# Optimization experiments

Measured on AMD Instinct MI355X. Metric: run time of the kernel, lower is better.

## Reference

```python
import jax, jax.numpy as jnp
import numpy as np

THETA0 = 3.0
THETA = 5.0


def _edt(bg):
    """Exact Euclidean distance transform.
    bg: [B,H,W] bool, True where distance is 0 (the 'background'/feature set).
    Returns [B,H,W] float32 distance of every pixel to the nearest True pixel.
    Separable two-pass algorithm: 1D pass along H via scan, then exact
    min over column offsets along W (Meijster lower-envelope done densely).
    """
    B, H, W = bg.shape
    big = jnp.float32(H + W)
    f = bg.astype(jnp.float32)
    xs = jnp.moveaxis(f, 1, 0)  # [H,B,W] scan over rows

    def step(carry, row):
        d = jnp.where(row > 0, 0.0, carry + 1.0)
        return d, d

    init = jnp.full((B, W), big, jnp.float32)
    _, gf = jax.lax.scan(step, init, xs)                  # top-down
    _, gb = jax.lax.scan(step, init, xs, reverse=True)    # bottom-up
    g = jnp.minimum(gf, gb)            # [H,B,W] 1D vertical distance
    g = jnp.moveaxis(g, 0, 1)          # [B,H,W]
    g2 = jnp.minimum(g, big) ** 2
    col = jnp.arange(W, dtype=jnp.float32)
    off2 = (col[:, None] - col[None, :]) ** 2             # [j,k]
    # d2[b,i,j] = min_k g2[b,i,k] + (j-k)^2   -> [B,H,W,W] intermediate
    d2 = jnp.min(g2[:, :, None, :] + off2[None, None, :, :], axis=-1)
    return jnp.sqrt(d2)


def reference(predictions, targets):
    # predictions: [B,1,H,W] logits; targets: [B,1,H,W] binary masks
    t = targets[:, 0]                                   # [B,H,W]
    fg = t > 0.5
    dist_pos = _edt(~fg)   # distance_transform_edt(target): dist to nearest 0
    dist_neg = _edt(fg)    # distance_transform_edt(1-target): dist to nearest 1
    dist_map = jnp.where(fg, dist_pos, -dist_neg)
    # weight = 1 / (1 + exp((|d| - theta0)/theta)) == sigmoid(-(|d|-theta0)/theta)
    weight = jax.nn.sigmoid(-(jnp.abs(dist_map) - THETA0) / THETA)[:, None]  # [B,1,H,W]
    # numerically stable BCE-with-logits == BCE(sigmoid(x), t)
    x = predictions
    bce = jnp.maximum(x, 0.0) - x * targets + jnp.log1p(jnp.exp(-jnp.abs(x)))
    return jnp.mean(bce * weight)


def setup_inputs() -> dict:
    key = jax.random.key(0)
    k1, k2 = jax.random.split(key)
    B, C, H, W = 8, 1, 256, 256
    predictions = jax.random.normal(k1, (B, C, H, W), dtype=jnp.float32)
    targets = jax.random.randint(k2, (B, C, H, W), 0, 2).astype(jnp.float32)
    return {"predictions": predictions, "targets": targets}
```

## Files before the change

kernel.cpp:

```cpp
#include <hip/hip_runtime.h>
#include <math.h>

#define BB 8
#define HH 256
#define WW 256
#define NPIX (BB*HH*WW)
#define BIGI 512
#define BIGBIG (1<<20)

#define P_OFF   (2 * NPIX)
#define P_STRIDE 32
#define C_OFF   (P_OFF + 16 * P_STRIDE)

__global__ __launch_bounds__(512) void pack_masks_t(
    const float* __restrict__ tgt,
    float* __restrict__ ws) {
  __shared__ unsigned int halfw[2][8][32];

  if (blockIdx.x == 0) {
    if (threadIdx.x < 16) ws[P_OFF + threadIdx.x * P_STRIDE] = 0.0f;
    if (threadIdx.x == 16) ((int*)ws)[C_OFF] = 0;
  }

  int tid = threadIdx.x;
  int h = tid >> 8;
  int j = (tid >> 5) & 7;
  int c = tid & 31;
  int im = blockIdx.x >> 3;
  int w = ((blockIdx.x & 7) << 5) + c;
  size_t ib = (size_t)im * (HH * WW) + (size_t)(32 * j + 16 * h) * WW + w;

  unsigned int m = 0;
#pragma unroll
  for (int i = 0; i < 16; ++i) {
    float t = tgt[ib + (size_t)i * WW];
    m |= (t > 0.5f ? 1u : 0u) << i;
  }
  halfw[h][j][c] = m;
  __syncthreads();

  if (h == 0) {
    unsigned int full = halfw[0][j][c] | (halfw[1][j][c] << 16);
    ((unsigned int*)ws)[im * 2048 + w * 8 + j] = full;
  }
}

#define ENV_G(gg) { float4 v = s4[gg];                            \
    float D0 = fw - (float)((gg) << 2);                           \
    d2 = fminf(d2, fmaf(D0, D0, v.x));                            \
    float D1 = D0 - 1.0f; d2 = fminf(d2, fmaf(D1, D1, v.y));      \
    float D2 = D0 - 2.0f; d2 = fminf(d2, fmaf(D2, D2, v.z));      \
    float D3 = D0 - 3.0f; d2 = fminf(d2, fmaf(D3, D3, v.w)); }

__global__ __launch_bounds__(1024) void edt_row_loss5(
    const float* __restrict__ pred,
    float* __restrict__ ws,
    float* __restrict__ out) {
  __shared__ __align__(16) float lA[4][WW];
  __shared__ __align__(16) float lB[4][WW];
  __shared__ float wsum[16];
  __shared__ int lastFlag;

  const unsigned int* maskws = (const unsigned int*)ws;
  float* partials = ws + P_OFF;
  int* counter = ((int*)ws) + C_OFF;

  int tid = threadIdx.x;
  int im = blockIdx.x >> 6;
  int rg = blockIdx.x & 63;
  int r = tid >> 8;
  int w = tid & 255;
  int R = 4 * rg + r;
  int k = R >> 5;
  int rr = R & 31;

  const uint4* mp = (const uint4*)(maskws + im * 2048 + w * 8);
  uint4 mlo = mp[0], mhi = mp[1];
  unsigned int M[8] = {mlo.x, mlo.y, mlo.z, mlo.w, mhi.x, mhi.y, mhi.z, mhi.w};

  float x = pred[(size_t)blockIdx.x * (4 * WW) + tid];

  int fcA = BIGBIG, fcB = BIGBIG, bcA = BIGBIG, bcB = BIGBIG;
  {
    int cA = BIGBIG, cB = BIGBIG;
#pragma unroll
    for (int j = 0; j < 8; ++j) {
      if (j == k) { fcA = cA; fcB = cB; }
      unsigned int a = ~M[j], bm = M[j];
      cA = a  ? (int)__builtin_clz(a)  : cA + 32;
      cB = bm ? (int)__builtin_clz(bm) : cB + 32;
    }
  }
  {
    int cA = BIGBIG, cB = BIGBIG;
#pragma unroll
    for (int j = 7; j >= 0; --j) {
      if (j == k) { bcA = cA; bcB = cB; }
      unsigned int a = ~M[j], bm = M[j];
      cA = a  ? (int)__builtin_ctz(a)  : cA + 32;
      cB = bm ? (int)__builtin_ctz(bm) : cB + 32;
    }
  }

  unsigned int mk = M[k];
  bool fg = (mk >> rr) & 1u;
  float t = fg ? 1.0f : 0.0f;

  {
    unsigned int mA = ~mk;
    unsigned int xx = mA << (31 - rr);
    unsigned int yy = mA >> rr;
    int df = xx ? (int)__builtin_clz(xx) : (rr + 1 + fcA);
    int db = yy ? (int)__builtin_ctz(yy) : (32 - rr + bcA);
    int d = min(min(df, db), BIGI);
    lA[r][w] = (float)(d * d);
  }
  {
    unsigned int xx = mk << (31 - rr);
    unsigned int yy = mk >> rr;
    int df = xx ? (int)__builtin_clz(xx) : (rr + 1 + fcB);
    int db = yy ? (int)__builtin_ctz(yy) : (32 - rr + bcB);
    int d = min(min(df, db), BIGI);
    lB[r][w] = (float)(d * d);
  }
  __syncthreads();

  const float4* s4 = (const float4*)(fg ? lA[r] : lB[r]);
  int gc = w >> 2;
  float fw = (float)w;
  float d2 = 1e30f;

  ENV_G(gc);
  for (int dlt = 1; dlt <= 16; ++dlt) {
    int gl = gc - dlt, gr = gc + dlt;
    int bl = (gl >= 0) ? (w - 4 * gl - 3) : 100000;
    int br = (gr <= 63) ? (4 * gr - w) : 100000;
    int bb = min(bl, br);
    float bb2 = (float)bb * (float)bb;
    if (__all(d2 <= bb2)) break;
    if (gl >= 0) ENV_G(gl);
    if (gr <= 63) ENV_G(gr);
  }

  float dd = sqrtf(d2);
  float weight = 1.0f / (1.0f + __expf((dd - 3.0f) * 0.2f));
  float bce = fmaxf(x, 0.0f) - x * t + log1pf(__expf(-fabsf(x)));
  float c = bce * weight * (1.0f / (float)NPIX);

#pragma unroll
  for (int off = 32; off > 0; off >>= 1) c += __shfl_down(c, off, 64);
  if ((tid & 63) == 0) wsum[tid >> 6] = c;
  __syncthreads();

  if (tid < 64) {
    float v = (tid < 16) ? wsum[tid] : 0.0f;
#pragma unroll
    for (int off = 8; off > 0; off >>= 1) v += __shfl_down(v, off, 64);
    if (tid == 0) {
      atomicAdd(&partials[(blockIdx.x & 15) * P_STRIDE], v);
      __threadfence();
      int done = atomicAdd(counter, 1);
      lastFlag = (done == (int)gridDim.x - 1) ? 1 : 0;
    }
  }
  __syncthreads();

  if (lastFlag && tid < 64) {
    float v = (tid < 16) ? atomicAdd(&partials[tid * P_STRIDE], 0.0f) : 0.0f;
#pragma unroll
    for (int off = 8; off > 0; off >>= 1) v += __shfl_down(v, off, 64);
    if (tid == 0) out[0] = v;
  }
}

extern "C" void kernel_launch(void* const* d_in, const int* in_sizes, int n_in,
                              void* d_out, int out_size, void* d_ws, size_t ws_size,
                              hipStream_t stream) {
  const float* pred = (const float*)d_in[0];
  const float* tgt  = (const float*)d_in[1];
  float* out = (float*)d_out;
  float* ws  = (float*)d_ws;

  pack_masks_t<<<dim3(64), dim3(512), 0, stream>>>(tgt, ws);
  edt_row_loss5<<<dim3(512), dim3(1024), 0, stream>>>(pred, ws, out);
}
```

Baseline: 69.90 us.

## Process four rows per thread in EDT kernel and widen mask packing grid

The EDT/loss kernel now has each thread handle four rows of one column, using 512-thread blocks and half as many blocks, so the per-column mask scans and loads are amortised across four rows and there is more independent work per thread. The packing kernel splits each 32-row word into four 8-row chunks across twice as many blocks to raise parallelism on the target reads. The cost is more registers per thread and fewer total threads, and the early-exit vote now waits for all four rows, which can add envelope iterations.

```diff
diff --git a/kernel.cpp b/kernel.cpp
--- a/kernel.cpp
+++ b/kernel.cpp
@@ -12,10 +12,10 @@
 #define P_STRIDE 32
 #define C_OFF   (P_OFF + 16 * P_STRIDE)
 
-__global__ __launch_bounds__(512) void pack_masks_t(
+__global__ __launch_bounds__(512) void pack_masks_t2(
     const float* __restrict__ tgt,
     float* __restrict__ ws) {
-  __shared__ unsigned int halfw[2][8][32];
+  __shared__ unsigned int chunk[4][4][32];
 
   if (blockIdx.x == 0) {
     if (threadIdx.x < 16) ws[P_OFF + threadIdx.x * P_STRIDE] = 0.0f;
@@ -23,42 +23,49 @@
   }
 
   int tid = threadIdx.x;
-  int h = tid >> 8;
-  int j = (tid >> 5) & 7;
-  int c = tid & 31;
-  int im = blockIdx.x >> 3;
-  int w = ((blockIdx.x & 7) << 5) + c;
-  size_t ib = (size_t)im * (HH * WW) + (size_t)(32 * j + 16 * h) * WW + w;
+  int c  = tid & 31;
+  int jl = (tid >> 5) & 3;
+  int h  = tid >> 7;
+  int im = blockIdx.x >> 4;
+  int tl = (blockIdx.x >> 1) & 7;
+  int v  = blockIdx.x & 1;
+  int j  = 4 * v + jl;
+  int w  = (tl << 5) + c;
+  size_t ib = (size_t)im * (HH * WW) + (size_t)(32 * j + 8 * h) * WW + w;
 
   unsigned int m = 0;
 #pragma unroll
-  for (int i = 0; i < 16; ++i) {
+  for (int i = 0; i < 8; ++i) {
     float t = tgt[ib + (size_t)i * WW];
     m |= (t > 0.5f ? 1u : 0u) << i;
   }
-  halfw[h][j][c] = m;
+  chunk[h][jl][c] = m;
   __syncthreads();
 
   if (h == 0) {
-    unsigned int full = halfw[0][j][c] | (halfw[1][j][c] << 16);
+    unsigned int full = chunk[0][jl][c] | (chunk[1][jl][c] << 8) |
+                        (chunk[2][jl][c] << 16) | (chunk[3][jl][c] << 24);
     ((unsigned int*)ws)[im * 2048 + w * 8 + j] = full;
   }
 }
 
-#define ENV_G(gg) { float4 v = s4[gg];                            \
-    float D0 = fw - (float)((gg) << 2);                           \
-    d2 = fminf(d2, fmaf(D0, D0, v.x));                            \
-    float D1 = D0 - 1.0f; d2 = fminf(d2, fmaf(D1, D1, v.y));      \
-    float D2 = D0 - 2.0f; d2 = fminf(d2, fmaf(D2, D2, v.z));      \
-    float D3 = D0 - 3.0f; d2 = fminf(d2, fmaf(D3, D3, v.w)); }
-
-__global__ __launch_bounds__(1024) void edt_row_loss5(
+__device__ __forceinline__ void env4(const float4* __restrict__ s4, int gg,
+                                     float fw, float& d2) {
+  float4 v = s4[gg];
+  float D0 = fw - (float)(gg << 2);
+  d2 = fminf(d2, fmaf(D0, D0, v.x));
+  float D1 = D0 - 1.0f; d2 = fminf(d2, fmaf(D1, D1, v.y));
+  float D2 = D0 - 2.0f; d2 = fminf(d2, fmaf(D2, D2, v.z));
+  float D3 = D0 - 3.0f; d2 = fminf(d2, fmaf(D3, D3, v.w));
+}
+
+__global__ __launch_bounds__(512) void edt_row_loss7(
     const float* __restrict__ pred,
     float* __restrict__ ws,
     float* __restrict__ out) {
-  __shared__ __align__(16) float lA[4][WW];
-  __shared__ __align__(16) float lB[4][WW];
-  __shared__ float wsum[16];
+  __shared__ __align__(16) float lA[8][WW];
+  __shared__ __align__(16) float lB[8][WW];
+  __shared__ float wsum[8];
   __shared__ int lastFlag;
 
   const unsigned int* maskws = (const unsigned int*)ws;
@@ -66,26 +73,34 @@
   int* counter = ((int*)ws) + C_OFF;
 
   int tid = threadIdx.x;
-  int im = blockIdx.x >> 6;
-  int rg = blockIdx.x & 63;
+  int bid = blockIdx.x;
+  int im = bid >> 5;
+  int rg = bid & 31;
   int r = tid >> 8;
   int w = tid & 255;
-  int R = 4 * rg + r;
-  int k = R >> 5;
-  int rr = R & 31;
+  int R0 = 8 * rg + 4 * r;
+
+  int kq[4], rq[4];
+#pragma unroll
+  for (int p = 0; p < 4; ++p) { kq[p] = (R0 + p) >> 5; rq[p] = (R0 + p) & 31; }
 
   const uint4* mp = (const uint4*)(maskws + im * 2048 + w * 8);
   uint4 mlo = mp[0], mhi = mp[1];
   unsigned int M[8] = {mlo.x, mlo.y, mlo.z, mlo.w, mhi.x, mhi.y, mhi.z, mhi.w};
 
-  float x = pred[(size_t)blockIdx.x * (4 * WW) + tid];
-
-  int fcA = BIGBIG, fcB = BIGBIG, bcA = BIGBIG, bcB = BIGBIG;
+  size_t pb = (size_t)bid * 2048 + (size_t)r * 1024 + w;
+  float x[4];
+#pragma unroll
+  for (int p = 0; p < 4; ++p) x[p] = pred[pb + (size_t)(p << 8)];
+
+  int fcA[4], fcB[4], bcA[4], bcB[4];
   {
     int cA = BIGBIG, cB = BIGBIG;
 #pragma unroll
     for (int j = 0; j < 8; ++j) {
-      if (j == k) { fcA = cA; fcB = cB; }
+#pragma unroll
+      for (int p = 0; p < 4; ++p)
+        if (j == kq[p]) { fcA[p] = cA; fcB[p] = cB; }
       unsigned int a = ~M[j], bm = M[j];
       cA = a  ? (int)__builtin_clz(a)  : cA + 32;
       cB = bm ? (int)__builtin_clz(bm) : cB + 32;
@@ -95,57 +110,78 @@
     int cA = BIGBIG, cB = BIGBIG;
 #pragma unroll
     for (int j = 7; j >= 0; --j) {
-      if (j == k) { bcA = cA; bcB = cB; }
+#pragma unroll
+      for (int p = 0; p < 4; ++p)
+        if (j == kq[p]) { bcA[p] = cA; bcB[p] = cB; }
       unsigned int a = ~M[j], bm = M[j];
       cA = a  ? (int)__builtin_ctz(a)  : cA + 32;
       cB = bm ? (int)__builtin_ctz(bm) : cB + 32;
     }
   }
 
-  unsigned int mk = M[k];
-  bool fg = (mk >> rr) & 1u;
-  float t = fg ? 1.0f : 0.0f;
-
-  {
-    unsigned int mA = ~mk;
-    unsigned int xx = mA << (31 - rr);
-    unsigned int yy = mA >> rr;
-    int df = xx ? (int)__builtin_clz(xx) : (rr + 1 + fcA);
-    int db = yy ? (int)__builtin_ctz(yy) : (32 - rr + bcA);
-    int d = min(min(df, db), BIGI);
-    lA[r][w] = (float)(d * d);
-  }
-  {
-    unsigned int xx = mk << (31 - rr);
-    unsigned int yy = mk >> rr;
-    int df = xx ? (int)__builtin_clz(xx) : (rr + 1 + fcB);
-    int db = yy ? (int)__builtin_ctz(yy) : (32 - rr + bcB);
-    int d = min(min(df, db), BIGI);
-    lB[r][w] = (float)(d * d);
-  }
-  __syncthreads();
-
-  const float4* s4 = (const float4*)(fg ? lA[r] : lB[r]);
+  bool fg[4]; float t[4];
+#pragma unroll
+  for (int p = 0; p < 4; ++p) {
+    unsigned int mk = M[kq[p]];
+    int rr = rq[p];
+    fg[p] = (mk >> rr) & 1u;
+    t[p] = fg[p] ? 1.0f : 0.0f;
+    {
+      unsigned int mA = ~mk;
+      unsigned int xx = mA << (31 - rr), yy = mA >> rr;
+      int df = xx ? (int)__builtin_clz(xx) : (rr + 1 + fcA[p]);
+      int db = yy ? (int)__builtin_ctz(yy) : (32 - rr + bcA[p]);
+      int d = min(min(df, db), BIGI);
+      lA[(r << 2) + p][w] = (float)(d * d);
+    }
+    {
+      unsigned int xx = mk << (31 - rr), yy = mk >> rr;
+      int df = xx ? (int)__builtin_clz(xx) : (rr + 1 + fcB[p]);
+      int db = yy ? (int)__builtin_ctz(yy) : (32 - rr + bcB[p]);
+      int d = min(min(df, db), BIGI);
+      lB[(r << 2) + p][w] = (float)(d * d);
+    }
+  }
+  __syncthreads();
+
+  const float4* s4[4];
+  float d2[4] = {1e30f, 1e30f, 1e30f, 1e30f};
+#pragma unroll
+  for (int p = 0; p < 4; ++p)
+    s4[p] = (const float4*)(fg[p] ? lA[(r << 2) + p] : lB[(r << 2) + p]);
+
   int gc = w >> 2;
   float fw = (float)w;
-  float d2 = 1e30f;
-
-  ENV_G(gc);
+#pragma unroll
+  for (int p = 0; p < 4; ++p) env4(s4[p], gc, fw, d2[p]);
+
   for (int dlt = 1; dlt <= 16; ++dlt) {
     int gl = gc - dlt, gr = gc + dlt;
     int bl = (gl >= 0) ? (w - 4 * gl - 3) : 100000;
     int br = (gr <= 63) ? (4 * gr - w) : 100000;
     int bb = min(bl, br);
     float bb2 = (float)bb * (float)bb;
-    if (__all(d2 <= bb2)) break;
-    if (gl >= 0) ENV_G(gl);
-    if (gr <= 63) ENV_G(gr);
-  }
-
-  float dd = sqrtf(d2);
-  float weight = 1.0f / (1.0f + __expf((dd - 3.0f) * 0.2f));
-  float bce = fmaxf(x, 0.0f) - x * t + log1pf(__expf(-fabsf(x)));
-  float c = bce * weight * (1.0f / (float)NPIX);
+    if (__all(d2[0] <= bb2 && d2[1] <= bb2 && d2[2] <= bb2 && d2[3] <= bb2))
+      break;
+    if (gl >= 0) {
+#pragma unroll
+      for (int p = 0; p < 4; ++p) env4(s4[p], gl, fw, d2[p]);
+    }
+    if (gr <= 63) {
+#pragma unroll
+      for (int p = 0; p < 4; ++p) env4(s4[p], gr, fw, d2[p]);
+    }
+  }
+
+  float c = 0.0f;
+#pragma unroll
+  for (int p = 0; p < 4; ++p) {
+    float dd = sqrtf(d2[p]);
+    float wt = 1.0f / (1.0f + __expf((dd - 3.0f) * 0.2f));
+    float bce = fmaxf(x[p], 0.0f) - x[p] * t[p] + log1pf(__expf(-fabsf(x[p])));
+    c += bce * wt;
+  }
+  c *= (1.0f / (float)NPIX);
 
 #pragma unroll
   for (int off = 32; off > 0; off >>= 1) c += __shfl_down(c, off, 64);
@@ -153,11 +189,11 @@
   __syncthreads();
 
   if (tid < 64) {
-    float v = (tid < 16) ? wsum[tid] : 0.0f;
-#pragma unroll
-    for (int off = 8; off > 0; off >>= 1) v += __shfl_down(v, off, 64);
+    float v = (tid < 8) ? wsum[tid] : 0.0f;
+#pragma unroll
+    for (int off = 4; off > 0; off >>= 1) v += __shfl_down(v, off, 64);
     if (tid == 0) {
-      atomicAdd(&partials[(blockIdx.x & 15) * P_STRIDE], v);
+      atomicAdd(&partials[(bid & 15) * P_STRIDE], v);
       __threadfence();
       int done = atomicAdd(counter, 1);
       lastFlag = (done == (int)gridDim.x - 1) ? 1 : 0;
@@ -181,6 +217,6 @@
   float* out = (float*)d_out;
   float* ws  = (float*)d_ws;
 
-  pack_masks_t<<<dim3(64), dim3(512), 0, stream>>>(tgt, ws);
-  edt_row_loss5<<<dim3(512), dim3(1024), 0, stream>>>(pred, ws, out);
-}
+  pack_masks_t2<<<dim3(128), dim3(512), 0, stream>>>(tgt, ws);
+  edt_row_loss7<<<dim3(256), dim3(512), 0, stream>>>(pred, ws, out);
+}
```

Measured after the change: 67.07 us. -4.1%, faster.
